# Kernel tuning notes

Hardware: AMD Instinct MI355X
Metric: run time of the kernel (lower is better)

## Reference

```python
import jax, jax.numpy as jnp
import numpy as np

N, E, H, D, C, L = 20000, 320000, 8, 64, 512, 2  # nodes, edges, heads, head_dim, channels, layers


def layer_norm(x, g, b, eps=1e-5):
    mu = x.mean(-1, keepdims=True)
    var = ((x - mu) ** 2).mean(-1, keepdims=True)
    return (x - mu) / jnp.sqrt(var + eps) * g + b


def setup_inputs() -> dict:
    key = jax.random.key(0)
    ks = jax.random.split(key, 14)
    s = 0.02
    x = jax.random.normal(ks[0], (N, C), jnp.float32)
    edge_index = jax.random.randint(ks[1], (2, E), 0, N, jnp.int32)
    edge_type = jax.random.randint(ks[2], (E,), 0, 10, jnp.int32)
    edge_repre = jax.random.normal(ks[3], (E,), jnp.float32)
    # Per-layer TransformerConv params (query/key/value/skip linears, each with bias)
    Wq = jax.random.normal(ks[4], (L, C, C), jnp.float32) * s
    Wk = jax.random.normal(ks[5], (L, C, C), jnp.float32) * s
    Wv = jax.random.normal(ks[6], (L, C, C), jnp.float32) * s
    Ws = jax.random.normal(ks[7], (L, C, C), jnp.float32) * s
    bq = jnp.zeros((L, C), jnp.float32)
    bk = jnp.zeros((L, C), jnp.float32)
    bv = jnp.zeros((L, C), jnp.float32)
    bs = jnp.zeros((L, C), jnp.float32)
    # FFN + shared LayerNorm
    W1 = jax.random.normal(ks[8], (C, 2 * C), jnp.float32) * s
    b1 = jnp.zeros((2 * C,), jnp.float32)
    W2 = jax.random.normal(ks[9], (2 * C, C), jnp.float32) * s
    b2 = jnp.zeros((C,), jnp.float32)
    ln_g = jnp.ones((C,), jnp.float32)
    ln_b = jnp.zeros((C,), jnp.float32)
    return {"x": x, "edge_index": edge_index, "edge_type": edge_type, "edge_repre": edge_repre,
            "Wq": Wq, "bq": bq, "Wk": Wk, "bk": bk, "Wv": Wv, "bv": bv, "Ws": Ws, "bs": bs,
            "W1": W1, "b1": b1, "W2": W2, "b2": b2, "ln_g": ln_g, "ln_b": ln_b}


def reference(x, edge_index, edge_type, edge_repre, Wq, bq, Wk, bk, Wv, bv, Ws, bs, W1, b1, W2, b2, ln_g, ln_b):
    src, dst = edge_index[0], edge_index[1]  # messages flow src -> dst (PyG source_to_target)
    enc = x
    scale = 1.0 / jnp.sqrt(jnp.float32(D))
    for l in range(L):
        q = (x @ Wq[l] + bq[l]).reshape(N, H, D)
        k = (x @ Wk[l] + bk[l]).reshape(N, H, D)
        v = (x @ Wv[l] + bv[l]).reshape(N, H, D)
        # per-edge attention logits [E, H]
        a = (q[dst] * k[src]).sum(-1) * scale
        # segment softmax over edges sharing a destination node
        amax = jax.ops.segment_max(a, dst, num_segments=N)
        amax = jnp.where(jnp.isfinite(amax), amax, 0.0)
        e = jnp.exp(a - amax[dst])
        denom = jax.ops.segment_sum(e, dst, num_segments=N)
        alpha = e / (denom[dst] + 1e-16)
        # scatter-aggregate weighted values, concat heads
        agg = jax.ops.segment_sum(alpha[:, :, None] * v[src], dst, num_segments=N).reshape(N, C)
        # root/skip connection (beta=False) + module-level residual to enc_emb
        x = agg + (x @ Ws[l] + bs[l]) + enc
    x = layer_norm(x, ln_g, ln_b)
    x = (jax.nn.relu(x @ W1 + b1) @ W2 + b2) + x
    x = layer_norm(x, ln_g, ln_b)
    return x + enc
```

## Files before the change

### kernel.cpp

```cpp
#include <hip/hip_runtime.h>

typedef __attribute__((ext_vector_type(8))) short short8;
typedef __attribute__((ext_vector_type(4))) float f32x4;

__device__ __forceinline__ unsigned short f2b(float f){
  union { float f; unsigned u; } x; x.f = f;
  unsigned r = x.u + 0x7fffu + ((x.u >> 16) & 1u);
  return (unsigned short)(r >> 16);
}
__device__ __forceinline__ float b2f(unsigned short v){
  union { unsigned u; float f; } x; x.u = ((unsigned)v) << 16; return x.f;
}

__device__ __forceinline__ unsigned char enc1(float v){
#if __has_builtin(__builtin_amdgcn_cvt_pk_fp8_f32)
  return (unsigned char)(__builtin_amdgcn_cvt_pk_fp8_f32(v, v, 0, false) & 0xff);
#else
  union{float f;unsigned u;}x; x.f=v;
  unsigned s = x.u >> 31;
  float av = fabsf(v);
  if (av >= 448.f) return (unsigned char)((s<<7)|0x7e);
  if (av < 0.0078125f){ unsigned d=(unsigned)(av*512.f+0.5f); return (unsigned char)((s<<7)|d); }
  unsigned q = x.u & 0x7fffffff;
  q = q + 0x7ffff + ((q>>20)&1);
  int e2 = (int)(q>>23) - 127;
  unsigned m3 = (q>>20)&7;
  if (e2 < -6){ unsigned d=(unsigned)(av*512.f+0.5f); return (unsigned char)((s<<7)|d); }
  return (unsigned char)((s<<7) | ((unsigned)(e2+7)<<3) | m3);
#endif
}
__device__ __forceinline__ void dec4(unsigned u, float* o){
#if __has_builtin(__builtin_amdgcn_cvt_pk_f32_fp8)
  auto lo = __builtin_amdgcn_cvt_pk_f32_fp8((int)u, false);
  auto hi = __builtin_amdgcn_cvt_pk_f32_fp8((int)u, true);
  o[0]=lo[0]; o[1]=lo[1]; o[2]=hi[0]; o[3]=hi[1];
#else
  #pragma unroll
  for (int j=0;j<4;j++){
    unsigned b = (u >> (8*j)) & 0xffu;
    unsigned s = b >> 7, ex = (b >> 3) & 15u, mn = b & 7u;
    union{unsigned u;float f;} x;
    x.u = ex ? ((s<<31)|((ex+120u)<<23)|(mn<<20)) : (s<<31);
    o[j] = x.f;
  }
#endif
}

__global__ void count_k(const int* __restrict__ dst, int* __restrict__ deg, int E){
  int e = blockIdx.x*256 + threadIdx.x;
  if (e < E) atomicAdd(&deg[dst[e]], 1);
}

__global__ void scan_k(const int* __restrict__ deg, int* __restrict__ rowstart,
                       int* __restrict__ cursor, int n)
{
  __shared__ int wsum[16];
  int tid = threadIdx.x, lane = tid & 63, wv = tid >> 6;
  int CH = (n + 1023) >> 10;
  int b0 = tid * CH; if (b0 > n) b0 = n;
  int bend = b0 + CH; if (bend > n) bend = n;
  int sum = 0;
  for (int i = b0; i < bend; ++i) sum += deg[i];
  int xs = sum;
  #pragma unroll
  for (int o=1;o<64;o<<=1){ int t = __shfl_up(xs, o, 64); if (lane >= o) xs += t; }
  if (lane == 63) wsum[wv] = xs;
  __syncthreads();
  if (tid < 16){
    int w = wsum[tid];
    #pragma unroll
    for (int o=1;o<16;o<<=1){ int t = __shfl_up(w, o, 64); if (tid >= o) w += t; }
    wsum[tid] = w;
  }
  __syncthreads();
  int off = (wv ? wsum[wv-1] : 0) + xs - sum;
  int run = off;
  for (int i = b0; i < bend; ++i){ rowstart[i] = run; cursor[i] = run; run += deg[i]; }
  if (b0 < n && bend == n) rowstart[n] = run;
  if (n == 0 && tid == 0) rowstart[0] = 0;
}

__global__ void fill_k(const int* __restrict__ src, const int* __restrict__ dst,
                       int* __restrict__ cursor, int* __restrict__ csrc, int E){
  int e = blockIdx.x*256 + threadIdx.x;
  if (e < E){
    int p = atomicAdd(&cursor[dst[e]], 1);
    csrc[p] = src[e];
  }
}

__global__ void transpose_all_k(const float* __restrict__ Wq, const float* __restrict__ Wk,
  const float* __restrict__ Wv, const float* __restrict__ Ws,
  const float* __restrict__ W1, const float* __restrict__ W2,
  unsigned short* __restrict__ wtqkvs, unsigned short* __restrict__ wt1,
  unsigned short* __restrict__ wt2)
{
  int bid = blockIdx.x;
  const float* src; unsigned short* dst; int r, c, lb;
  if (bid < 1024){
    int j = bid >> 7;
    int l = j >> 2, w = j & 3;
    src = (w==0?Wq : w==1?Wk : w==2?Wv : Ws) + (size_t)l*512*512;
    dst = wtqkvs + (size_t)l*2048*512 + (size_t)w*512*512;
    r = 512; c = 512; lb = bid & 127;
  } else if (bid < 1280){ src = W1; dst = wt1; r = 512; c = 1024; lb = bid - 1024; }
  else { src = W2; dst = wt2; r = 1024; c = 512; lb = bid - 1280; }
  int idx = lb*256 + threadIdx.x;
  int o = idx % c;
  int i0 = (idx / c) << 3;
  short8 vv;
  #pragma unroll
  for (int j=0;j<8;j++) ((unsigned short*)&vv)[j] = f2b(src[(size_t)(i0+j)*c + o]);
  *(short8*)&dst[(size_t)o*r + i0] = vv;
}

__global__ void cvt2_k(const float* __restrict__ in, unsigned short* __restrict__ out1,
                       unsigned short* __restrict__ out2, size_t n){
  size_t i = ((size_t)blockIdx.x*256 + threadIdx.x)*8;
  if (i >= n) return;
  const float4* p = (const float4*)(in + i);
  float4 a0 = p[0], a1 = p[1];
  short8 vv;
  ((unsigned short*)&vv)[0] = f2b(a0.x); ((unsigned short*)&vv)[1] = f2b(a0.y);
  ((unsigned short*)&vv)[2] = f2b(a0.z); ((unsigned short*)&vv)[3] = f2b(a0.w);
  ((unsigned short*)&vv)[4] = f2b(a1.x); ((unsigned short*)&vv)[5] = f2b(a1.y);
  ((unsigned short*)&vv)[6] = f2b(a1.z); ((unsigned short*)&vv)[7] = f2b(a1.w);
  *(short8*)&out1[i] = vv;
  *(short8*)&out2[i] = vv;
}

template<int MODE, int KC, int NN>
__global__ __launch_bounds__(256) void gemm_k(
    const unsigned short* __restrict__ A,
    const unsigned short* __restrict__ Bt,
    int M,
    const float* __restrict__ bias0, const float* __restrict__ bias1,
    const float* __restrict__ bias2, const float* __restrict__ bias3,
    unsigned short* __restrict__ outB, unsigned short* __restrict__ outB2,
    unsigned char* __restrict__ outC,
    float* __restrict__ outF, const float* __restrict__ res)
{
  __shared__ unsigned short lA[2][128*64];
  __shared__ unsigned short lB[2][128*64];
  const int tid  = threadIdx.x;
  const int lane = tid & 63;
  const int wid  = tid >> 6;

  const int nwg = gridDim.x;
  int id = blockIdx.x;
  int q = nwg >> 3, r = nwg & 7;
  int xc = id & 7, yy = id >> 3;
  int swz = (xc < r ? xc*(q+1) : r*(q+1) + (xc-r)*q) + yy;
  const int bm = (swz / NN) * 128;
  const int bn = (swz % NN) * 128;
  const int wm = (wid >> 1) * 64;
  const int wn = (wid & 1) * 64;

  f32x4 acc[4][4];
  #pragma unroll
  for (int m=0;m<4;m++)
    #pragma unroll
    for (int n=0;n<4;n++) acc[m][n] = (f32x4)0.f;

  constexpr int NT = KC / 64;

  auto STAGE = [&](int buf, int kt){
    #pragma unroll
    for (int it = 0; it < 4; ++it) {
      int chunk = it*256 + tid;
      int row = chunk >> 3;
      int cin = chunk & 7;
      int scol = (cin ^ (row & 7)) * 8;
      int ga = bm + row; if (ga >= M) ga = M - 1;
      __builtin_amdgcn_global_load_lds(
        (const __attribute__((address_space(1))) void*)(A + (size_t)ga * KC + kt + scol),
        (__attribute__((address_space(3))) void*)(&lA[buf][(it*256 + (wid<<6)) * 8]),
        16, 0, 0);
      __builtin_amdgcn_global_load_lds(
        (const __attribute__((address_space(1))) void*)(Bt + (size_t)(bn + row) * KC + kt + scol),
        (__attribute__((address_space(3))) void*)(&lB[buf][(it*256 + (wid<<6)) * 8]),
        16, 0, 0);
    }
  };

  auto COMPUTE = [&](int buf){
    #pragma unroll
    for (int ks = 0; ks < 2; ++ks) {
      short8 af[4], bfr[4];
      #pragma unroll
      for (int m=0;m<4;m++){
        int rr = wm + m*16 + (lane & 15);
        int ch = (ks*4 + (lane >> 4)) ^ (rr & 7);
        af[m] = *(const short8*)&lA[buf][rr*64 + ch*8];
      }
      #pragma unroll
      for (int n=0;n<4;n++){
        int rr = wn + n*16 + (lane & 15);
        int ch = (ks*4 + (lane >> 4)) ^ (rr & 7);
        bfr[n] = *(const short8*)&lB[buf][rr*64 + ch*8];
      }
      #pragma unroll
      for (int m=0;m<4;m++)
        #pragma unroll
        for (int n=0;n<4;n++)
          acc[m][n] = __builtin_amdgcn_mfma_f32_16x16x32_bf16(af[m], bfr[n], acc[m][n], 0,0,0);
    }
  };

  STAGE(0, 0);
  if (NT > 1) STAGE(1, 64);
  #pragma unroll
  for (int t = 0; t < NT; ++t){
    if (t == NT-1) asm volatile("s_waitcnt vmcnt(0)" ::: "memory");
    else           asm volatile("s_waitcnt vmcnt(8)" ::: "memory");
    __builtin_amdgcn_s_barrier();
    COMPUTE(t & 1);
    asm volatile("s_waitcnt lgkmcnt(0)" ::: "memory");
    __builtin_amdgcn_s_barrier();
    if (t + 2 < NT) STAGE(t & 1, (t+2)*64);
  }

  #pragma unroll
  for (int m=0;m<4;m++){
    int row0 = bm + wm + m*16 + ((lane >> 4) << 2);
    #pragma unroll
    for (int n=0;n<4;n++){
      int col = bn + wn + n*16 + (lane & 15);
      float bval;
      if (MODE == 0){
        bval = (col < 512) ? bias0[col]
             : (col < 1024) ? bias1[col-512]
             : (col < 1536) ? bias2[col-1024] : bias3[col-1536];
      } else {
        bval = bias0[col];
      }
      #pragma unroll
      for (int r4=0;r4<4;r4++){
        int row = row0 + r4;
        if (row < M){
          float v = acc[m][n][r4] + bval;
          if (MODE == 0){
            if (col < 512)       outB[(size_t)row*512 + col] = f2b(v);
            else if (col < 1536) outC[(size_t)row*1024 + (col-512)] = enc1(v);
            else                 outB2[(size_t)row*512 + (col-1536)] = f2b(v);
          } else if (MODE == 1){
            v = fmaxf(v, 0.0f);
            outB[(size_t)row*(NN*128) + col] = f2b(v);
          } else {
            v += res[(size_t)row*512 + col];
            outF[(size_t)row*512 + col] = v;
          }
        }
      }
    }
  }
}

template<int WF32>
__global__ __launch_bounds__(256) void attn_k(
  const unsigned short* __restrict__ qb, const unsigned char* __restrict__ kv8,
  const unsigned short* __restrict__ skipb, const unsigned short* __restrict__ encb,
  const int* __restrict__ rowstart, const int* __restrict__ csrc,
  float* __restrict__ xout, unsigned short* __restrict__ xoutb, int N)
{
  int n = blockIdx.x*4 + (threadIdx.x>>6);
  if (n >= N) return;
  int lane = threadIdx.x & 63;
  const short8 qv = *(const short8*)&qb[(size_t)n*512 + lane*8];
  float qf[8];
  #pragma unroll
  for (int j=0;j<8;j++) qf[j] = b2f(((const unsigned short*)&qv)[j]);
  float m = -__builtin_inff(), l = 0.f;
  float acc[8] = {0.f,0.f,0.f,0.f,0.f,0.f,0.f,0.f};
  int e = rowstart[n], e1 = rowstart[n+1];
  if (e < e1){
    int s = csrc[e];
    uint2 kc = *(const uint2*)&kv8[(size_t)s*1024 + lane*8];
    uint2 vc = *(const uint2*)&kv8[(size_t)s*1024 + 512 + lane*8];
    for (; e < e1; ++e){
      int sn = (e+1 < e1) ? csrc[e+1] : s;
      uint2 kn = *(const uint2*)&kv8[(size_t)sn*1024 + lane*8];
      uint2 vn = *(const uint2*)&kv8[(size_t)sn*1024 + 512 + lane*8];
      float kf[8]; dec4(kc.x, kf); dec4(kc.y, kf+4);
      float dot = 0.f;
      #pragma unroll
      for (int j=0;j<8;j++) dot += qf[j]*kf[j];
      dot += __shfl_xor(dot,1); dot += __shfl_xor(dot,2); dot += __shfl_xor(dot,4);
      float a = dot * 0.125f;
      float mn2 = fmaxf(m, a);
      float corr = __expf(m - mn2);
      float p = __expf(a - mn2);
      l = l*corr + p;
      float vf[8]; dec4(vc.x, vf); dec4(vc.y, vf+4);
      #pragma unroll
      for (int j=0;j<8;j++) acc[j] = acc[j]*corr + p*vf[j];
      m = mn2;
      kc = kn; vc = vn;
    }
  }
  float inv = 1.f/(l + 1e-16f);
  size_t base = (size_t)n*512 + (size_t)lane*8;
  const short8 sv = *(const short8*)&skipb[base];
  const short8 ev = *(const short8*)&encb[base];
  short8 ob;
  #pragma unroll
  for (int j=0;j<8;j++){
    float o = acc[j]*inv + b2f(((const unsigned short*)&sv)[j]) + b2f(((const unsigned short*)&ev)[j]);
    if (WF32) xout[base+j] = o;
    ((unsigned short*)&ob)[j] = f2b(o);
  }
  *(short8*)&xoutb[base] = ob;
}

template<int MODE>
__global__ __launch_bounds__(256) void ln_k(const float* __restrict__ x,
  const float* __restrict__ g, const float* __restrict__ b,
  float* __restrict__ outF, unsigned short* __restrict__ outB,
  const float* __restrict__ addv, int N)
{
  int n = blockIdx.x*4 + (threadIdx.x>>6);
  if (n >= N) return;
  int lane = threadIdx.x & 63;
  size_t base = (size_t)n*512 + (size_t)lane*8;
  const float4* p = (const float4*)(x + base);
  float4 a0 = p[0], a1 = p[1];
  float v[8] = {a0.x,a0.y,a0.z,a0.w,a1.x,a1.y,a1.z,a1.w};
  float s=0.f, ss=0.f;
  #pragma unroll
  for (int j=0;j<8;j++){ s += v[j]; ss += v[j]*v[j]; }
  #pragma unroll
  for (int o=1;o<64;o<<=1){ s += __shfl_xor(s,o); ss += __shfl_xor(ss,o); }
  float mean = s * (1.f/512.f);
  float var  = ss * (1.f/512.f) - mean*mean;
  float rstd = rsqrtf(var + 1e-5f);
  #pragma unroll
  for (int j=0;j<8;j++){
    int c = lane*8 + j;
    float o = (v[j]-mean)*rstd*g[c] + b[c];
    if (MODE == 0){ outF[base+j] = o; outB[base+j] = f2b(o); }
    else          { outF[base+j] = o + addv[base+j]; }
  }
}

extern "C" void kernel_launch(void* const* d_in, const int* in_sizes, int n_in,
                              void* d_out, int out_size, void* d_ws, size_t ws_size,
                              hipStream_t stream)
{
  const float* x0  = (const float*)d_in[0];
  const int*  eidx = (const int*)d_in[1];
  const float* Wq  = (const float*)d_in[4];
  const float* bq  = (const float*)d_in[5];
  const float* Wk  = (const float*)d_in[6];
  const float* bk  = (const float*)d_in[7];
  const float* Wv  = (const float*)d_in[8];
  const float* bv  = (const float*)d_in[9];
  const float* Wsk = (const float*)d_in[10];
  const float* bs  = (const float*)d_in[11];
  const float* W1  = (const float*)d_in[12];
  const float* b1  = (const float*)d_in[13];
  const float* W2  = (const float*)d_in[14];
  const float* b2  = (const float*)d_in[15];
  const float* lng = (const float*)d_in[16];
  const float* lnb = (const float*)d_in[17];

  const int N = in_sizes[0] / 512;
  const int E = in_sizes[1] / 2;
  const int* esrc = eidx;
  const int* edst = eidx + E;

  char* ws = (char*)d_ws;
  size_t off = 0;
  auto alloc = [&](size_t bytes)->char*{
    char* p = ws + off; off = (off + bytes + 255) & ~(size_t)255; return p;
  };
  unsigned short* wtqkvs = (unsigned short*)alloc((size_t)2*2048*512*2);
  unsigned short* wt1    = (unsigned short*)alloc((size_t)1024*512*2);
  unsigned short* wt2    = (unsigned short*)alloc((size_t)512*1024*2);
  unsigned short* qb     = (unsigned short*)alloc((size_t)N*512*2);
  unsigned char*  kv8    = (unsigned char*)alloc((size_t)N*1024);
  float*          skip   = (float*)alloc((size_t)N*512*4);
  float*          xbuf   = (float*)alloc((size_t)N*512*4);
  unsigned short* xb     = (unsigned short*)alloc((size_t)N*512*2);
  unsigned short* encb   = (unsigned short*)alloc((size_t)N*512*2);
  unsigned short* skipb  = (unsigned short*)alloc((size_t)N*512*2);
  int* deg      = (int*)alloc((size_t)N*4);
  int* rowstart = (int*)alloc((size_t)(N+1)*4);
  int* cursor   = (int*)alloc((size_t)N*4);
  int* csrc     = (int*)alloc((size_t)E*4);
  unsigned short* tbuf = qb;

  hipMemsetAsync(deg, 0, (size_t)N*4, stream);
  count_k<<<(E+255)/256, 256, 0, stream>>>(edst, deg, E);
  scan_k<<<1, 1024, 0, stream>>>(deg, rowstart, cursor, N);
  fill_k<<<(E+255)/256, 256, 0, stream>>>(esrc, edst, cursor, csrc, E);

  transpose_all_k<<<1536, 256, 0, stream>>>(Wq, Wk, Wv, Wsk, W1, W2, wtqkvs, wt1, wt2);

  const int cvtBlocks = (int)(((size_t)N*512/8 + 255)/256);
  const int rowBlocks = (N + 3)/4;
  const int MB = (N + 127)/128;

  cvt2_k<<<cvtBlocks, 256, 0, stream>>>(x0, xb, encb, (size_t)N*512);
  for (int l = 0; l < 2; ++l){
    gemm_k<0,512,16><<<MB*16, 256, 0, stream>>>(xb, wtqkvs + (size_t)l*2048*512, N,
        bq + l*512, bk + l*512, bv + l*512, bs + l*512, qb, skipb, kv8, nullptr, nullptr);
    if (l == 0)
      attn_k<0><<<rowBlocks, 256, 0, stream>>>(qb, kv8, skipb, encb, rowstart, csrc, nullptr, xb, N);
    else
      attn_k<1><<<rowBlocks, 256, 0, stream>>>(qb, kv8, skipb, encb, rowstart, csrc, xbuf, xb, N);
  }

  ln_k<0><<<rowBlocks, 256, 0, stream>>>(xbuf, lng, lnb, skip, xb, nullptr, N);
  gemm_k<1,512,8><<<MB*8, 256, 0, stream>>>(xb, wt1, N,
      b1, nullptr, nullptr, nullptr, tbuf, nullptr, nullptr, nullptr, nullptr);
  gemm_k<2,1024,4><<<MB*4, 256, 0, stream>>>(tbuf, wt2, N,
      b2, nullptr, nullptr, nullptr, nullptr, nullptr, nullptr, xbuf, skip);
  ln_k<1><<<rowBlocks, 256, 0, stream>>>(xbuf, lng, lnb, (float*)d_out, nullptr, x0, N);
}
```

Before: 552.1 us.

## Single-buffer GEMM LDS, add occupancy hint, shrink M tile for FFN2

Replaces the double-buffered LDS pipeline in the GEMM with a single buffer and plain load/sync/compute/sync per K-step, which halves LDS use. It adds a launch-bounds occupancy hint of 5 blocks and makes the M-tile size a template parameter, using 64-row tiles for the second FFN GEMM so it launches more blocks. The trade is losing overlap of global loads with MFMA compute in exchange for more resident waves and better load balance.

```diff
diff --git a/kernel.cpp b/kernel.cpp
--- a/kernel.cpp
+++ b/kernel.cpp
@@ -129,8 +129,8 @@
   *(short8*)&out2[i] = vv;
 }
 
-template<int MODE, int KC, int NN>
-__global__ __launch_bounds__(256) void gemm_k(
+template<int MODE, int KC, int NN, int MF>
+__global__ __launch_bounds__(256, 5) void gemm_k(
     const unsigned short* __restrict__ A,
     const unsigned short* __restrict__ Bt,
     int M,
@@ -140,8 +140,9 @@
     unsigned char* __restrict__ outC,
     float* __restrict__ outF, const float* __restrict__ res)
 {
-  __shared__ unsigned short lA[2][128*64];
-  __shared__ unsigned short lB[2][128*64];
+  constexpr int BM = MF*32;
+  __shared__ unsigned short lA[BM*64];
+  __shared__ unsigned short lB[128*64];
   const int tid  = threadIdx.x;
   const int lane = tid & 63;
   const int wid  = tid >> 6;
@@ -151,22 +152,22 @@
   int q = nwg >> 3, r = nwg & 7;
   int xc = id & 7, yy = id >> 3;
   int swz = (xc < r ? xc*(q+1) : r*(q+1) + (xc-r)*q) + yy;
-  const int bm = (swz / NN) * 128;
+  const int bm = (swz / NN) * BM;
   const int bn = (swz % NN) * 128;
-  const int wm = (wid >> 1) * 64;
+  const int wm = (wid >> 1) * (MF*16);
   const int wn = (wid & 1) * 64;
 
-  f32x4 acc[4][4];
-  #pragma unroll
-  for (int m=0;m<4;m++)
+  f32x4 acc[MF][4];
+  #pragma unroll
+  for (int m=0;m<MF;m++)
     #pragma unroll
     for (int n=0;n<4;n++) acc[m][n] = (f32x4)0.f;
 
   constexpr int NT = KC / 64;
 
-  auto STAGE = [&](int buf, int kt){
-    #pragma unroll
-    for (int it = 0; it < 4; ++it) {
+  for (int kt = 0; kt < KC; kt += 64){
+    #pragma unroll
+    for (int it = 0; it < MF; ++it){
       int chunk = it*256 + tid;
       int row = chunk >> 3;
       int cin = chunk & 7;
@@ -174,54 +175,47 @@
       int ga = bm + row; if (ga >= M) ga = M - 1;
       __builtin_amdgcn_global_load_lds(
         (const __attribute__((address_space(1))) void*)(A + (size_t)ga * KC + kt + scol),
-        (__attribute__((address_space(3))) void*)(&lA[buf][(it*256 + (wid<<6)) * 8]),
+        (__attribute__((address_space(3))) void*)(&lA[(it*256 + (wid<<6)) * 8]),
         16, 0, 0);
+    }
+    #pragma unroll
+    for (int it = 0; it < 4; ++it){
+      int chunk = it*256 + tid;
+      int row = chunk >> 3;
+      int cin = chunk & 7;
+      int scol = (cin ^ (row & 7)) * 8;
       __builtin_amdgcn_global_load_lds(
         (const __attribute__((address_space(1))) void*)(Bt + (size_t)(bn + row) * KC + kt + scol),
-        (__attribute__((address_space(3))) void*)(&lB[buf][(it*256 + (wid<<6)) * 8]),
+        (__attribute__((address_space(3))) void*)(&lB[(it*256 + (wid<<6)) * 8]),
         16, 0, 0);
     }
-  };
-
-  auto COMPUTE = [&](int buf){
-    #pragma unroll
-    for (int ks = 0; ks < 2; ++ks) {
-      short8 af[4], bfr[4];
-      #pragma unroll
-      for (int m=0;m<4;m++){
+    __syncthreads();
+    #pragma unroll
+    for (int ks = 0; ks < 2; ++ks){
+      short8 af[MF], bfr[4];
+      #pragma unroll
+      for (int m=0;m<MF;m++){
         int rr = wm + m*16 + (lane & 15);
         int ch = (ks*4 + (lane >> 4)) ^ (rr & 7);
-        af[m] = *(const short8*)&lA[buf][rr*64 + ch*8];
+        af[m] = *(const short8*)&lA[rr*64 + ch*8];
       }
       #pragma unroll
       for (int n=0;n<4;n++){
         int rr = wn + n*16 + (lane & 15);
         int ch = (ks*4 + (lane >> 4)) ^ (rr & 7);
-        bfr[n] = *(const short8*)&lB[buf][rr*64 + ch*8];
+        bfr[n] = *(const short8*)&lB[rr*64 + ch*8];
       }
       #pragma unroll
-      for (int m=0;m<4;m++)
+      for (int m=0;m<MF;m++)
         #pragma unroll
         for (int n=0;n<4;n++)
           acc[m][n] = __builtin_amdgcn_mfma_f32_16x16x32_bf16(af[m], bfr[n], acc[m][n], 0,0,0);
     }
-  };
-
-  STAGE(0, 0);
-  if (NT > 1) STAGE(1, 64);
-  #pragma unroll
-  for (int t = 0; t < NT; ++t){
-    if (t == NT-1) asm volatile("s_waitcnt vmcnt(0)" ::: "memory");
-    else           asm volatile("s_waitcnt vmcnt(8)" ::: "memory");
-    __builtin_amdgcn_s_barrier();
-    COMPUTE(t & 1);
-    asm volatile("s_waitcnt lgkmcnt(0)" ::: "memory");
-    __builtin_amdgcn_s_barrier();
-    if (t + 2 < NT) STAGE(t & 1, (t+2)*64);
-  }
-
-  #pragma unroll
-  for (int m=0;m<4;m++){
+    __syncthreads();
+  }
+
+  #pragma unroll
+  for (int m=0;m<MF;m++){
     int row0 = bm + wm + m*16 + ((lane >> 4) << 2);
     #pragma unroll
     for (int n=0;n<4;n++){
@@ -398,11 +392,12 @@
 
   const int cvtBlocks = (int)(((size_t)N*512/8 + 255)/256);
   const int rowBlocks = (N + 3)/4;
-  const int MB = (N + 127)/128;
+  const int MB4 = (N + 127)/128;
+  const int MB2 = (N + 63)/64;
 
   cvt2_k<<<cvtBlocks, 256, 0, stream>>>(x0, xb, encb, (size_t)N*512);
   for (int l = 0; l < 2; ++l){
-    gemm_k<0,512,16><<<MB*16, 256, 0, stream>>>(xb, wtqkvs + (size_t)l*2048*512, N,
+    gemm_k<0,512,16,4><<<MB4*16, 256, 0, stream>>>(xb, wtqkvs + (size_t)l*2048*512, N,
         bq + l*512, bk + l*512, bv + l*512, bs + l*512, qb, skipb, kv8, nullptr, nullptr);
     if (l == 0)
       attn_k<0><<<rowBlocks, 256, 0, stream>>>(qb, kv8, skipb, encb, rowstart, csrc, nullptr, xb, N);
@@ -411,9 +406,9 @@
   }
 
   ln_k<0><<<rowBlocks, 256, 0, stream>>>(xbuf, lng, lnb, skip, xb, nullptr, N);
-  gemm_k<1,512,8><<<MB*8, 256, 0, stream>>>(xb, wt1, N,
+  gemm_k<1,512,8,4><<<MB4*8, 256, 0, stream>>>(xb, wt1, N,
       b1, nullptr, nullptr, nullptr, tbuf, nullptr, nullptr, nullptr, nullptr);
-  gemm_k<2,1024,4><<<MB*4, 256, 0, stream>>>(tbuf, wt2, N,
+  gemm_k<2,1024,4,2><<<MB2*4, 256, 0, stream>>>(tbuf, wt2, N,
       b2, nullptr, nullptr, nullptr, nullptr, nullptr, nullptr, xbuf, skip);
   ln_k<1><<<rowBlocks, 256, 0, stream>>>(xbuf, lng, lnb, (float*)d_out, nullptr, x0, N);
 }
```

New measurement: 652.5 us. 18.2% more time.

## Run QKV/skip projection GEMMs in FP8 with scaled weights

Applied to the files above, without the earlier changes.

Adds an FP8 MFMA GEMM for the per-layer fused Q/K/V/skip projection. Weights are pre-scaled by 64 before FP8 conversion, and the scale is undone in the epilogue. The input activations and the layer-0 attention output are now written as FP8 instead of bf16, which halves the A and B operand traffic and raises MFMA throughput. The cost is lower precision in the projections, with accuracy risk from FP8 quantization of activations and weights.

```diff
diff --git a/kernel.cpp b/kernel.cpp
--- a/kernel.cpp
+++ b/kernel.cpp
@@ -29,6 +29,15 @@
   return (unsigned char)((s<<7) | ((unsigned)(e2+7)<<3) | m3);
 #endif
 }
+__device__ __forceinline__ unsigned pk4(float a,float b,float c,float d){
+#if __has_builtin(__builtin_amdgcn_cvt_pk_fp8_f32)
+  int v = __builtin_amdgcn_cvt_pk_fp8_f32(a, b, 0, false);
+  v = __builtin_amdgcn_cvt_pk_fp8_f32(c, d, v, true);
+  return (unsigned)v;
+#else
+  return (unsigned)enc1(a) | ((unsigned)enc1(b)<<8) | ((unsigned)enc1(c)<<16) | ((unsigned)enc1(d)<<24);
+#endif
+}
 __device__ __forceinline__ void dec4(unsigned u, float* o){
 #if __has_builtin(__builtin_amdgcn_cvt_pk_f32_fp8)
   auto lo = __builtin_amdgcn_cvt_pk_f32_fp8((int)u, false);
@@ -92,18 +101,29 @@
 __global__ void transpose_all_k(const float* __restrict__ Wq, const float* __restrict__ Wk,
   const float* __restrict__ Wv, const float* __restrict__ Ws,
   const float* __restrict__ W1, const float* __restrict__ W2,
-  unsigned short* __restrict__ wtqkvs, unsigned short* __restrict__ wt1,
+  unsigned char* __restrict__ wtqkvs8, unsigned short* __restrict__ wt1,
   unsigned short* __restrict__ wt2)
 {
   int bid = blockIdx.x;
-  const float* src; unsigned short* dst; int r, c, lb;
   if (bid < 1024){
     int j = bid >> 7;
     int l = j >> 2, w = j & 3;
-    src = (w==0?Wq : w==1?Wk : w==2?Wv : Ws) + (size_t)l*512*512;
-    dst = wtqkvs + (size_t)l*2048*512 + (size_t)w*512*512;
-    r = 512; c = 512; lb = bid & 127;
-  } else if (bid < 1280){ src = W1; dst = wt1; r = 512; c = 1024; lb = bid - 1024; }
+    const float* src = (w==0?Wq : w==1?Wk : w==2?Wv : Ws) + (size_t)l*512*512;
+    unsigned char* dst = wtqkvs8 + ((size_t)l*2048 + (size_t)w*512)*512;
+    int idx = (bid & 127)*256 + threadIdx.x;
+    int o = idx & 511;
+    int i0 = (idx >> 9) << 3;
+    float v[8];
+    #pragma unroll
+    for (int t=0;t<8;t++) v[t] = 64.f * src[(size_t)(i0+t)*512 + o];
+    unsigned lo = pk4(v[0],v[1],v[2],v[3]);
+    unsigned hi = pk4(v[4],v[5],v[6],v[7]);
+    unsigned long long pk = (unsigned long long)lo | ((unsigned long long)hi << 32);
+    *(unsigned long long*)&dst[(size_t)o*512 + i0] = pk;
+    return;
+  }
+  const float* src; unsigned short* dst; int r, c, lb;
+  if (bid < 1280){ src = W1; dst = wt1; r = 512; c = 1024; lb = bid - 1024; }
   else { src = W2; dst = wt2; r = 1024; c = 512; lb = bid - 1280; }
   int idx = lb*256 + threadIdx.x;
   int o = idx % c;
@@ -114,8 +134,8 @@
   *(short8*)&dst[(size_t)o*r + i0] = vv;
 }
 
-__global__ void cvt2_k(const float* __restrict__ in, unsigned short* __restrict__ out1,
-                       unsigned short* __restrict__ out2, size_t n){
+__global__ void cvt8_k(const float* __restrict__ in, unsigned char* __restrict__ out8,
+                       unsigned short* __restrict__ outb, size_t n){
   size_t i = ((size_t)blockIdx.x*256 + threadIdx.x)*8;
   if (i >= n) return;
   const float4* p = (const float4*)(in + i);
@@ -125,8 +145,124 @@
   ((unsigned short*)&vv)[2] = f2b(a0.z); ((unsigned short*)&vv)[3] = f2b(a0.w);
   ((unsigned short*)&vv)[4] = f2b(a1.x); ((unsigned short*)&vv)[5] = f2b(a1.y);
   ((unsigned short*)&vv)[6] = f2b(a1.z); ((unsigned short*)&vv)[7] = f2b(a1.w);
-  *(short8*)&out1[i] = vv;
-  *(short8*)&out2[i] = vv;
+  *(short8*)&outb[i] = vv;
+  unsigned lo = pk4(a0.x,a0.y,a0.z,a0.w);
+  unsigned hi = pk4(a1.x,a1.y,a1.z,a1.w);
+  *(unsigned long long*)&out8[i] = (unsigned long long)lo | ((unsigned long long)hi<<32);
+}
+
+__global__ __launch_bounds__(256) void gemm8f_k(
+    const unsigned char* __restrict__ A8,
+    const unsigned char* __restrict__ Bt8,
+    int M,
+    const float* __restrict__ bias0, const float* __restrict__ bias1,
+    const float* __restrict__ bias2, const float* __restrict__ bias3,
+    unsigned short* __restrict__ qb, unsigned short* __restrict__ skipb,
+    unsigned char* __restrict__ kv8)
+{
+  __shared__ unsigned char lA[2][128*128];
+  __shared__ unsigned char lB[2][128*128];
+  const int tid  = threadIdx.x;
+  const int lane = tid & 63;
+  const int wid  = tid >> 6;
+
+  const int nwg = gridDim.x;
+  int id = blockIdx.x;
+  int q = nwg >> 3, r = nwg & 7;
+  int xc = id & 7, yy = id >> 3;
+  int swz = (xc < r ? xc*(q+1) : r*(q+1) + (xc-r)*q) + yy;
+  const int bm = (swz >> 4) * 128;
+  const int bn = (swz & 15) * 128;
+  const int wm = (wid >> 1) * 64;
+  const int wn = (wid & 1) * 64;
+
+  f32x4 acc[4][4];
+  #pragma unroll
+  for (int m=0;m<4;m++)
+    #pragma unroll
+    for (int n=0;n<4;n++) acc[m][n] = (f32x4)0.f;
+
+  auto STAGE = [&](int buf, int kt){
+    #pragma unroll
+    for (int it = 0; it < 4; ++it) {
+      int chunk = it*256 + tid;
+      int row = chunk >> 3;
+      int cin = chunk & 7;
+      int scol = (cin ^ (row & 7)) * 16;
+      int ga = bm + row; if (ga >= M) ga = M - 1;
+      __builtin_amdgcn_global_load_lds(
+        (const __attribute__((address_space(1))) void*)(A8 + (size_t)ga*512 + kt + scol),
+        (__attribute__((address_space(3))) void*)(&lA[buf][(it*256 + (wid<<6))*16]),
+        16, 0, 0);
+      __builtin_amdgcn_global_load_lds(
+        (const __attribute__((address_space(1))) void*)(Bt8 + (size_t)(bn + row)*512 + kt + scol),
+        (__attribute__((address_space(3))) void*)(&lB[buf][(it*256 + (wid<<6))*16]),
+        16, 0, 0);
+    }
+  };
+
+  const int kq  = lane >> 4;
+  const int ofs = (kq & 1) * 8;
+  const int ch2 = kq >> 1;
+  auto COMPUTE = [&](int buf){
+    #pragma unroll
+    for (int s = 0; s < 4; ++s){
+      unsigned long long af[4], bfr[4];
+      #pragma unroll
+      for (int m=0;m<4;m++){
+        int rr = wm + m*16 + (lane & 15);
+        int c  = (s*2 + ch2) ^ (rr & 7);
+        af[m] = *(const unsigned long long*)&lA[buf][rr*128 + c*16 + ofs];
+      }
+      #pragma unroll
+      for (int n=0;n<4;n++){
+        int rr = wn + n*16 + (lane & 15);
+        int c  = (s*2 + ch2) ^ (rr & 7);
+        bfr[n] = *(const unsigned long long*)&lB[buf][rr*128 + c*16 + ofs];
+      }
+      #pragma unroll
+      for (int m=0;m<4;m++)
+        #pragma unroll
+        for (int n=0;n<4;n++)
+          acc[m][n] = __builtin_amdgcn_mfma_f32_16x16x32_fp8_fp8(
+              (long)af[m], (long)bfr[n], acc[m][n], 0,0,0);
+    }
+  };
+
+  STAGE(0, 0);
+  STAGE(1, 128);
+  #pragma unroll
+  for (int t = 0; t < 4; ++t){
+    if (t == 3) asm volatile("s_waitcnt vmcnt(0)" ::: "memory");
+    else        asm volatile("s_waitcnt vmcnt(8)" ::: "memory");
+    __builtin_amdgcn_s_barrier();
+    COMPUTE(t & 1);
+    asm volatile("s_waitcnt lgkmcnt(0)" ::: "memory");
+    __builtin_amdgcn_s_barrier();
+    if (t + 2 < 4) STAGE(t & 1, (t+2)*128);
+  }
+
+  #pragma unroll
+  for (int m=0;m<4;m++){
+    int row0 = bm + wm + m*16 + ((lane >> 4) << 2);
+    #pragma unroll
+    for (int n=0;n<4;n++){
+      int col = bn + wn + n*16 + (lane & 15);
+      float bval = (col < 512) ? bias0[col]
+                 : (col < 1024) ? bias1[col-512]
+                 : (col < 1536) ? bias2[col-1024] : bias3[col-1536];
+      #pragma unroll
+      for (int r4=0;r4<4;r4++){
+        int row = row0 + r4;
+        if (row < M){
+          float v = acc[m][n][r4] * 0.015625f + bval;
+          if (col < 512)       qb[(size_t)row*512 + col] = f2b(v);
+          else if (col < 1536) kv8[(size_t)row*1024 + (col-512)] = enc1(v);
+          else                 skipb[(size_t)row*512 + (col-1536)] = f2b(v);
+        }
+      }
+    }
+  }
 }
 
 template<int MODE, int KC, int NN>
@@ -134,10 +270,8 @@
     const unsigned short* __restrict__ A,
     const unsigned short* __restrict__ Bt,
     int M,
-    const float* __restrict__ bias0, const float* __restrict__ bias1,
-    const float* __restrict__ bias2, const float* __restrict__ bias3,
-    unsigned short* __restrict__ outB, unsigned short* __restrict__ outB2,
-    unsigned char* __restrict__ outC,
+    const float* __restrict__ bias0,
+    unsigned short* __restrict__ outB,
     float* __restrict__ outF, const float* __restrict__ res)
 {
   __shared__ unsigned short lA[2][128*64];
@@ -226,24 +360,13 @@
     #pragma unroll
     for (int n=0;n<4;n++){
       int col = bn + wn + n*16 + (lane & 15);
-      float bval;
-      if (MODE == 0){
-        bval = (col < 512) ? bias0[col]
-             : (col < 1024) ? bias1[col-512]
-             : (col < 1536) ? bias2[col-1024] : bias3[col-1536];
-      } else {
-        bval = bias0[col];
-      }
+      float bval = bias0[col];
       #pragma unroll
       for (int r4=0;r4<4;r4++){
         int row = row0 + r4;
         if (row < M){
           float v = acc[m][n][r4] + bval;
-          if (MODE == 0){
-            if (col < 512)       outB[(size_t)row*512 + col] = f2b(v);
-            else if (col < 1536) outC[(size_t)row*1024 + (col-512)] = enc1(v);
-            else                 outB2[(size_t)row*512 + (col-1536)] = f2b(v);
-          } else if (MODE == 1){
+          if (MODE == 1){
             v = fmaxf(v, 0.0f);
             outB[(size_t)row*(NN*128) + col] = f2b(v);
           } else {
@@ -256,12 +379,12 @@
   }
 }
 
-template<int WF32>
+template<int OUT>
 __global__ __launch_bounds__(256) void attn_k(
   const unsigned short* __restrict__ qb, const unsigned char* __restrict__ kv8,
   const unsigned short* __restrict__ skipb, const unsigned short* __restrict__ encb,
   const int* __restrict__ rowstart, const int* __restrict__ csrc,
-  float* __restrict__ xout, unsigned short* __restrict__ xoutb, int N)
+  float* __restrict__ xout, unsigned char* __restrict__ xout8, int N)
 {
   int n = blockIdx.x*4 + (threadIdx.x>>6);
   if (n >= N) return;
@@ -302,14 +425,19 @@
   size_t base = (size_t)n*512 + (size_t)lane*8;
   const short8 sv = *(const short8*)&skipb[base];
   const short8 ev = *(const short8*)&encb[base];
-  short8 ob;
-  #pragma unroll
-  for (int j=0;j<8;j++){
-    float o = acc[j]*inv + b2f(((const unsigned short*)&sv)[j]) + b2f(((const unsigned short*)&ev)[j]);
-    if (WF32) xout[base+j] = o;
-    ((unsigned short*)&ob)[j] = f2b(o);
-  }
-  *(short8*)&xoutb[base] = ob;
+  float o[8];
+  #pragma unroll
+  for (int j=0;j<8;j++)
+    o[j] = acc[j]*inv + b2f(((const unsigned short*)&sv)[j]) + b2f(((const unsigned short*)&ev)[j]);
+  if (OUT == 0){
+    unsigned lo = pk4(o[0],o[1],o[2],o[3]);
+    unsigned hi = pk4(o[4],o[5],o[6],o[7]);
+    *(unsigned long long*)&xout8[base] = (unsigned long long)lo | ((unsigned long long)hi<<32);
+  } else {
+    float4* po = (float4*)&xout[base];
+    po[0] = make_float4(o[0],o[1],o[2],o[3]);
+    po[1] = make_float4(o[4],o[5],o[6],o[7]);
+  }
 }
 
 template<int MODE>
@@ -373,16 +501,17 @@
   auto alloc = [&](size_t bytes)->char*{
     char* p = ws + off; off = (off + bytes + 255) & ~(size_t)255; return p;
   };
-  unsigned short* wtqkvs = (unsigned short*)alloc((size_t)2*2048*512*2);
-  unsigned short* wt1    = (unsigned short*)alloc((size_t)1024*512*2);
-  unsigned short* wt2    = (unsigned short*)alloc((size_t)512*1024*2);
-  unsigned short* qb     = (unsigned short*)alloc((size_t)N*512*2);
-  unsigned char*  kv8    = (unsigned char*)alloc((size_t)N*1024);
-  float*          skip   = (float*)alloc((size_t)N*512*4);
-  float*          xbuf   = (float*)alloc((size_t)N*512*4);
-  unsigned short* xb     = (unsigned short*)alloc((size_t)N*512*2);
-  unsigned short* encb   = (unsigned short*)alloc((size_t)N*512*2);
-  unsigned short* skipb  = (unsigned short*)alloc((size_t)N*512*2);
+  unsigned char*  wtqkvs8 = (unsigned char*)alloc((size_t)2*2048*512);
+  unsigned short* wt1     = (unsigned short*)alloc((size_t)1024*512*2);
+  unsigned short* wt2     = (unsigned short*)alloc((size_t)512*1024*2);
+  unsigned short* qb      = (unsigned short*)alloc((size_t)N*512*2);
+  unsigned char*  kv8     = (unsigned char*)alloc((size_t)N*1024);
+  float*          skip    = (float*)alloc((size_t)N*512*4);
+  float*          xbuf    = (float*)alloc((size_t)N*512*4);
+  unsigned short* xb      = (unsigned short*)alloc((size_t)N*512*2);
+  unsigned char*  xb8     = (unsigned char*)alloc((size_t)N*512);
+  unsigned short* encb    = (unsigned short*)alloc((size_t)N*512*2);
+  unsigned short* skipb   = (unsigned short*)alloc((size_t)N*512*2);
   int* deg      = (int*)alloc((size_t)N*4);
   int* rowstart = (int*)alloc((size_t)(N+1)*4);
   int* cursor   = (int*)alloc((size_t)N*4);
@@ -394,26 +523,24 @@
   scan_k<<<1, 1024, 0, stream>>>(deg, rowstart, cursor, N);
   fill_k<<<(E+255)/256, 256, 0, stream>>>(esrc, edst, cursor, csrc, E);
 
-  transpose_all_k<<<1536, 256, 0, stream>>>(Wq, Wk, Wv, Wsk, W1, W2, wtqkvs, wt1, wt2);
+  transpose_all_k<<<1536, 256, 0, stream>>>(Wq, Wk, Wv, Wsk, W1, W2, wtqkvs8, wt1, wt2);
 
   const int cvtBlocks = (int)(((size_t)N*512/8 + 255)/256);
   const int rowBlocks = (N + 3)/4;
   const int MB = (N + 127)/128;
 
-  cvt2_k<<<cvtBlocks, 256, 0, stream>>>(x0, xb, encb, (size_t)N*512);
+  cvt8_k<<<cvtBlocks, 256, 0, stream>>>(x0, xb8, encb, (size_t)N*512);
   for (int l = 0; l < 2; ++l){
-    gemm_k<0,512,16><<<MB*16, 256, 0, stream>>>(xb, wtqkvs + (size_t)l*2048*512, N,
-        bq + l*512, bk + l*512, bv + l*512, bs + l*512, qb, skipb, kv8, nullptr, nullptr);
+    gemm8f_k<<<MB*16, 256, 0, stream>>>(xb8, wtqkvs8 + (size_t)l*2048*512, N,
+        bq + l*512, bk + l*512, bv + l*512, bs + l*512, qb, skipb, kv8);
     if (l == 0)
-      attn_k<0><<<rowBlocks, 256, 0, stream>>>(qb, kv8, skipb, encb, rowstart, csrc, nullptr, xb, N);
+      attn_k<0><<<rowBlocks, 256, 0, stream>>>(qb, kv8, skipb, encb, rowstart, csrc, nullptr, xb8, N);
     else
-      attn_k<1><<<rowBlocks, 256, 0, stream>>>(qb, kv8, skipb, encb, rowstart, csrc, xbuf, xb, N);
+      attn_k<1><<<rowBlocks, 256, 0, stream>>>(qb, kv8, skipb, encb, rowstart, csrc, xbuf, nullptr, N);
   }
 
   ln_k<0><<<rowBlocks, 256, 0, stream>>>(xbuf, lng, lnb, skip, xb, nullptr, N);
-  gemm_k<1,512,8><<<MB*8, 256, 0, stream>>>(xb, wt1, N,
-      b1, nullptr, nullptr, nullptr, tbuf, nullptr, nullptr, nullptr, nullptr);
-  gemm_k<2,1024,4><<<MB*4, 256, 0, stream>>>(tbuf, wt2, N,
-      b2, nullptr, nullptr, nullptr, nullptr, nullptr, nullptr, xbuf, skip);
+  gemm_k<1,512,8><<<MB*8, 256, 0, stream>>>(xb, wt1, N, b1, tbuf, nullptr, nullptr);
+  gemm_k<2,1024,4><<<MB*4, 256, 0, stream>>>(tbuf, wt2, N, b2, nullptr, xbuf, skip);
   ln_k<1><<<rowBlocks, 256, 0, stream>>>(xbuf, lng, lnb, (float*)d_out, nullptr, x0, N);
 }
```

Result: faster. 518.7 us (-6.1%).
